# Performance work log

Measured on AMD Instinct MI355X. Metric: run time of the kernel, lower is better.

## Reference

```python
import jax, jax.numpy as jnp
import numpy as np
from jax import lax

N_LAYERS = 10
N_BLOCKS = 3
N_STACK = N_LAYERS * N_BLOCKS  # 30
WIDTH = 512
SKIP_W = 256
CH = 1
QUANT = 256
BOTTLENECK = 16
KSIZE = 3
SCALE = 2 ** (N_LAYERS - 1)  # 512, nearest upsample factor
B, T = 1, 16384
T_EMB = T // SCALE  # 32


def causal_conv(x, w, b, dilation):
    # x: [B,Cin,T], w: [Cout,Cin,K] -> causal dilated conv, output [B,Cout,T]
    k = w.shape[-1]
    pad = (k - 1) * dilation
    y = lax.conv_general_dilated(x, w, window_strides=(1,), padding=[(pad, 0)],
                                 rhs_dilation=(dilation,),
                                 dimension_numbers=('NCH', 'OIH', 'NCH'))
    return y + b[None, :, None]


def conv1x1(x, w, b):
    # x: [B,Cin,T], w: [Cout,Cin]
    return jnp.einsum('oc,bct->bot', w, x) + b[None, :, None]


def setup_inputs() -> dict:
    key = jax.random.key(0)
    ks = jax.random.split(key, 24)
    s = 0.05
    inp = {
        'x': jax.random.normal(ks[0], (B, CH, T), jnp.float32),
        'embedding': jax.random.normal(ks[1], (B, BOTTLENECK, T_EMB), jnp.float32),
        'w_init': jax.random.normal(ks[2], (WIDTH, CH, KSIZE), jnp.float32) * s,
        'b_init': jnp.zeros((WIDTH,), jnp.float32),
        'w_iskip': jax.random.normal(ks[3], (SKIP_W, WIDTH), jnp.float32) * s,
        'b_iskip': jnp.zeros((SKIP_W,), jnp.float32),
        'w_dil': jax.random.normal(ks[4], (N_STACK, 2 * WIDTH, WIDTH, KSIZE), jnp.float32) * s,
        'b_dil': jnp.zeros((N_STACK, 2 * WIDTH), jnp.float32),
        'w_cond': jax.random.normal(ks[5], (N_STACK, 2 * WIDTH, BOTTLENECK), jnp.float32) * s,
        'b_cond': jnp.zeros((N_STACK, 2 * WIDTH), jnp.float32),
        'w_res': jax.random.normal(ks[6], (N_STACK, WIDTH, WIDTH), jnp.float32) * s,
        'b_res': jnp.zeros((N_STACK, WIDTH), jnp.float32),
        'w_skip': jax.random.normal(ks[7], (N_STACK, SKIP_W, WIDTH), jnp.float32) * s,
        'b_skip': jnp.zeros((N_STACK, SKIP_W), jnp.float32),
        'w_fskip': jax.random.normal(ks[8], (SKIP_W, SKIP_W), jnp.float32) * s,
        'b_fskip': jnp.zeros((SKIP_W,), jnp.float32),
        'w_fcond': jax.random.normal(ks[9], (SKIP_W, BOTTLENECK), jnp.float32) * s,
        'b_fcond': jnp.zeros((SKIP_W,), jnp.float32),
        'w_quant': jax.random.normal(ks[10], (QUANT, SKIP_W), jnp.float32) * s,
        'b_quant': jnp.zeros((QUANT,), jnp.float32),
    }
    return inp


def reference(x, embedding, w_init, b_init, w_iskip, b_iskip, w_dil, b_dil,
              w_cond, b_cond, w_res, b_res, w_skip, b_skip,
              w_fskip, b_fskip, w_fcond, b_fcond, w_quant, b_quant):
    # initial causal conv (kernel 3, dilation 1) + initial skip 1x1
    h = causal_conv(x, w_init, b_init, 1)            # [B,WIDTH,T]
    skip = conv1x1(h, w_iskip, b_iskip)              # [B,SKIP_W,T]
    for i in range(N_STACK):
        dilation = 2 ** (i % N_LAYERS)
        cond = conv1x1(embedding, w_cond[i], b_cond[i])      # [B,2W,T_EMB]
        cond_up = jnp.repeat(cond, SCALE, axis=-1)           # nearest upsample -> [B,2W,T]
        dilated = causal_conv(h, w_dil[i], b_dil[i], dilation) + cond_up
        filters = jax.nn.sigmoid(dilated[:, :WIDTH, :])
        gates = jnp.tanh(dilated[:, WIDTH:, :])
        pre = filters * gates
        h = h + conv1x1(pre, w_res[i], b_res[i])
        skip = skip + conv1x1(pre, w_skip[i], b_skip[i])
    skip = conv1x1(jax.nn.relu(skip), w_fskip, b_fskip)
    fcond = jnp.repeat(conv1x1(embedding, w_fcond, b_fcond), SCALE, axis=-1)
    skip = skip + fcond
    return conv1x1(jax.nn.relu(skip), w_quant, b_quant)     # [B,QUANT,T]
```

## Files before the change

kernel.cpp:

```cpp
#include <hip/hip_runtime.h>


typedef _Float16 f16x8 __attribute__((ext_vector_type(8)));
typedef float f32x4 __attribute__((ext_vector_type(4)));

#define NSTACK 30
#define TLEN   16384

typedef __attribute__((address_space(1))) const unsigned int glob_u32;
typedef __attribute__((address_space(3))) unsigned int lds_u32;

__device__ __forceinline__ void gll16(const unsigned short* g, unsigned short* l) {
  __builtin_amdgcn_global_load_lds((glob_u32*)g, (lds_u32*)l, 16, 0, 0);
}

__device__ __forceinline__ unsigned short f2h(float x) {
  union { _Float16 h; unsigned short u; } c;
  c.h = (_Float16)x;
  return c.u;
}
__device__ __forceinline__ unsigned pack2(float a, float b) {
  return (unsigned)f2h(a) | ((unsigned)f2h(b) << 16);
}
__device__ __forceinline__ float uplo(unsigned u){ union{unsigned v;_Float16 h[2];}c; c.v=u; return (float)c.h[0]; }
__device__ __forceinline__ float uphi(unsigned u){ union{unsigned v;_Float16 h[2];}c; c.v=u; return (float)c.h[1]; }
__device__ __forceinline__ f16x8 ldh(const unsigned short* p) {
  return *(const f16x8*)p;
}
__device__ __forceinline__ float sigmoidf_(float x){ return 1.0f/(1.0f+__expf(-x)); }
__device__ __forceinline__ float tanhf_(float x){ return 1.0f - 2.0f/(__expf(2.0f*x)+1.0f); }
#define MFMA16(a,b,c) __builtin_amdgcn_mfma_f32_16x16x32_f16((a),(b),(c),0,0,0)

#define SEG_T  15728640L
#define SEG_R  1966080L
#define SEG_S  983040L
#define SEG_I  32768L
#define SEG_F  16384L
#define SEG_Q  16384L
#define SEG_C  30976L
#define PREP_TOTAL (SEG_T+SEG_R+SEG_S+SEG_I+SEG_F+SEG_Q+SEG_C)

__device__ __forceinline__ void cast4(const float* src, unsigned short* dst, long g){
  f32x4 v = *(const f32x4*)(src + 4*g);
  unsigned int* d = (unsigned int*)(dst + 4*g);
  d[0] = pack2(v[0], v[1]);
  d[1] = pack2(v[2], v[3]);
}

__global__ void prep_kernel(
    const float* __restrict__ w_dil,  unsigned short* __restrict__ A_dil,
    const float* __restrict__ w_res,  unsigned short* __restrict__ Wres_h,
    const float* __restrict__ w_skip, unsigned short* __restrict__ Wskip_h,
    const float* __restrict__ w_iskip,unsigned short* __restrict__ Wiskip_h,
    const float* __restrict__ w_fskip,unsigned short* __restrict__ Wfskip_h,
    const float* __restrict__ w_quant,unsigned short* __restrict__ Wquant_h,
    const float* __restrict__ emb,
    const float* __restrict__ w_cond, const float* __restrict__ b_cond,
    const float* __restrict__ b_dil,
    const float* __restrict__ w_fcond,const float* __restrict__ b_fcond,
    float* __restrict__ cond_all, float* __restrict__ fcond_all) {
  long g = (long)blockIdx.x*256 + threadIdx.x;
  if (g < SEG_T) {
    int c = (int)(g & 511);
    int m = (int)((g >> 9) & 1023);
    int i = (int)(g >> 19);
    const float* s = w_dil + g*3;
    #pragma unroll
    for (int tap=0; tap<3; ++tap)
      A_dil[(((size_t)i*3+tap)*1024 + m)*512 + c] = f2h(s[tap]);
    return;
  }
  g -= SEG_T;
  if (g < SEG_R) { cast4(w_res,  Wres_h,  g); return; }
  g -= SEG_R;
  if (g < SEG_S) { cast4(w_skip, Wskip_h, g); return; }
  g -= SEG_S;
  if (g < SEG_I) { cast4(w_iskip, Wiskip_h, g); return; }
  g -= SEG_I;
  if (g < SEG_F) { cast4(w_fskip, Wfskip_h, g); return; }
  g -= SEG_F;
  if (g < SEG_Q) { cast4(w_quant, Wquant_h, g); return; }
  g -= SEG_Q;
  if (g < NSTACK*1024) {
    int row = (int)g;
    float acc[32];
    float base = b_cond[row] + b_dil[row];
    #pragma unroll
    for (int e=0;e<32;++e) acc[e] = base;
    #pragma unroll
    for (int c=0;c<16;++c) {
      float wv = w_cond[(size_t)row*16 + c];
      #pragma unroll
      for (int e=0;e<32;++e) acc[e] += wv * emb[c*32+e];
    }
    #pragma unroll
    for (int e=0;e<32;++e) cond_all[(size_t)row*32+e] = acc[e];
  } else if (g < NSTACK*1024 + 256) {
    int m = (int)(g - NSTACK*1024);
    float acc[32];
    float base = b_fcond[m];
    #pragma unroll
    for (int c=0;c<16;++c) {
      float wv = w_fcond[(size_t)m*16 + c];
      #pragma unroll
      for (int e=0;e<32;++e) acc[e] = (c==0 ? base : acc[e]) + wv * emb[c*32+e];
    }
    #pragma unroll
    for (int e=0;e<32;++e) fcond_all[(size_t)m*32+e] = acc[e];
  }
}

__global__ __launch_bounds__(512) void hs_kernel(
    const float* __restrict__ x, const float* __restrict__ w_init,
    const float* __restrict__ b_init,
    unsigned short* __restrict__ h_h16,
    const unsigned short* __restrict__ Wiskip,
    const float* __restrict__ b_iskip, unsigned short* __restrict__ skip16) {
  __shared__ unsigned short S[64][520];
  const int tid = threadIdx.x;
  const int tb = blockIdx.x << 6;

  for (int j = tid; j < 64*128; j += 512) {
    int r  = j >> 7;
    int c4 = (j & 127) << 2;
    int t  = tb + r;
    float xm2 = (t>=2)? x[t-2] : 0.f;
    float xm1 = (t>=1)? x[t-1] : 0.f;
    float x0  = x[t];
    float hv[4];
    #pragma unroll
    for (int q=0;q<4;++q) {
      int cc = c4 + q;
      hv[q] = w_init[cc*3+0]*xm2 + w_init[cc*3+1]*xm1 + w_init[cc*3+2]*x0 + b_init[cc];
    }
    unsigned p0 = pack2(hv[0],hv[1]), p1 = pack2(hv[2],hv[3]);
    unsigned int* hb = (unsigned int*)&h_h16[(size_t)t*512 + c4];
    hb[0] = p0; hb[1] = p1;
    unsigned int* sb = (unsigned int*)&S[r][c4];
    sb[0] = p0; sb[1] = p1;
  }
  __syncthreads();

  const int w = tid >> 6, l = tid & 63, lr = l & 15, lc = l >> 4;
  f32x4 acc[2][4];
  #pragma unroll
  for (int mf=0;mf<2;++mf)
    #pragma unroll
    for (int nf=0;nf<4;++nf) acc[mf][nf] = {0.f,0.f,0.f,0.f};
  for (int kc=0;kc<512;kc+=32) {
    f16x8 b[4];
    #pragma unroll
    for (int nf=0;nf<4;++nf)
      b[nf] = ldh(&S[16*nf+lr][kc + lc*8]);
    #pragma unroll
    for (int mf=0;mf<2;++mf) {
      f16x8 a = ldh(&Wiskip[(size_t)(w*32+16*mf+lr)*512 + kc + lc*8]);
      #pragma unroll
      for (int nf=0;nf<4;++nf)
        acc[mf][nf] = MFMA16(a, b[nf], acc[mf][nf]);
    }
  }
  #pragma unroll
  for (int mf=0;mf<2;++mf)
    #pragma unroll
    for (int nf=0;nf<4;++nf) {
      int s0 = w*32+16*mf+4*lc;
      int t  = tb+16*nf+lr;
      unsigned int* pp = (unsigned int*)&skip16[(size_t)t*256+s0];
      pp[0] = pack2(acc[mf][nf][0]+b_iskip[s0+0], acc[mf][nf][1]+b_iskip[s0+1]);
      pp[1] = pack2(acc[mf][nf][2]+b_iskip[s0+2], acc[mf][nf][3]+b_iskip[s0+3]);
    }
}

__global__ __launch_bounds__(512, 4) void dil_small_kernel(
    const unsigned short* __restrict__ h_in,
    unsigned short* __restrict__ pre,
    const unsigned short* __restrict__ A_dil,
    const float* __restrict__ cond,
    const unsigned short* __restrict__ zerobuf,
    int dilation) {
  __shared__ unsigned short Ab[2][128][32];
  __shared__ unsigned short Bb[2][384][32];
  const int tid = threadIdx.x;
  const int w = tid >> 6, l = tid & 63;
  const int lr = l & 15, lc = l >> 4;
  const int nt = blockIdx.x & 63, mt = blockIdx.x >> 6;
  const int tb = nt << 8;
  const int e  = tb >> 9;
  const int wr = w >> 2, wc = w & 3;

  const int srowA  = (w<<4) + (l>>2);
  const int srowB0 = w*48 + (l>>2);
  const int schunk = (l & 3) << 3;

  f32x4 fa[2][4], ga[2][4];
  #pragma unroll
  for (int mf=0;mf<2;++mf)
    #pragma unroll
    for (int nf=0;nf<4;++nf) { fa[mf][nf] = {0.f,0.f,0.f,0.f}; ga[mf][nf] = {0.f,0.f,0.f,0.f}; }

  auto stageA = [&](int buf, int s){
    const int kcc = s / 3;
    const int tap = s - kcc*3;
    const int kc  = kcc << 5;
    const int r = srowA;
    const int m = mt*64 + r + ((r>>6)*448);
    gll16(A_dil + (size_t)tap*(1024*512) + (size_t)m*512 + kc + schunk,
          &Ab[buf][(w<<4)][0]);
  };
  auto stageB = [&](int buf, int kcc){
    const int kc = kcc << 5;
    #pragma unroll
    for (int j=0;j<3;++j){
      const int r = srowB0 + j*16;
      const int t = tb + r - 128;
      const unsigned short* src = (t >= 0) ? (h_in + (size_t)t*512 + kc + schunk)
                                           : (zerobuf + schunk);
      gll16(src, &Bb[buf][w*48 + j*16][0]);
    }
  };

  stageA(0, 0);
  stageB(0, 0);
  for (int s=0; s<48; ++s) {
    const int curA = s & 1;
    const int kcc = s / 3;
    const int tap = s - kcc*3;
    const int curB = kcc & 1;
    __syncthreads();
    if (s+1 < 48) stageA(curA^1, s+1);
    if (tap == 2 && kcc+1 < 16) stageB(curB^1, kcc+1);
    const int shift = (2 - tap) * dilation;
    f16x8 af[2], ag[2], bf[4];
    #pragma unroll
    for (int mf=0;mf<2;++mf){
      const int row = (wr<<5) + (mf<<4) + lr;
      af[mf] = ldh(&Ab[curA][row][lc<<3]);
      ag[mf] = ldh(&Ab[curA][64+row][lc<<3]);
    }
    #pragma unroll
    for (int nf=0;nf<4;++nf){
      const int col = (wc<<6) + (nf<<4) + lr;
      bf[nf] = ldh(&Bb[curB][128 + col - shift][lc<<3]);
    }
    #pragma unroll
    for (int mf=0;mf<2;++mf)
      #pragma unroll
      for (int nf=0;nf<4;++nf){
        fa[mf][nf] = MFMA16(af[mf], bf[nf], fa[mf][nf]);
        ga[mf][nf] = MFMA16(ag[mf], bf[nf], ga[mf][nf]);
      }
  }

  #pragma unroll
  for (int mf=0;mf<2;++mf)
    #pragma unroll
    for (int nf=0;nf<4;++nf){
      const int m0 = mt*64 + (wr<<5) + (mf<<4) + (lc<<2);
      const int t  = tb + (wc<<6) + (nf<<4) + lr;
      float pv[4];
      #pragma unroll
      for (int r=0;r<4;++r){
        float f = fa[mf][nf][r] + cond[(size_t)(m0+r)*32 + e];
        float g = ga[mf][nf][r] + cond[(size_t)(m0+r+512)*32 + e];
        pv[r] = sigmoidf_(f) * tanhf_(g);
      }
      unsigned int* pp = (unsigned int*)&pre[(size_t)t*512 + m0];
      pp[0] = pack2(pv[0], pv[1]);
      pp[1] = pack2(pv[2], pv[3]);
    }
}

__global__ __launch_bounds__(512, 4) void dil_kernel(
    const unsigned short* __restrict__ h_in,
    unsigned short* __restrict__ pre,
    const unsigned short* __restrict__ A_dil,
    const float* __restrict__ cond,
    const unsigned short* __restrict__ zerobuf,
    int dilation) {
  __shared__ unsigned short Ab[2][128][32];
  __shared__ unsigned short Bb[2][256][32];
  const int tid = threadIdx.x;
  const int w = tid >> 6, l = tid & 63;
  const int lr = l & 15, lc = l >> 4;
  const int nt = blockIdx.x & 63, mt = blockIdx.x >> 6;
  const int tb = nt << 8;
  const int e  = tb >> 9;
  const int wr = w >> 2, wc = w & 3;

  const int srowA = (w<<4) + (l>>2);
  const int srowB0 = (w<<5) + (l>>2);
  const int schunk = (l & 3) << 3;

  f32x4 fa[2][4], ga[2][4];
  #pragma unroll
  for (int mf=0;mf<2;++mf)
    #pragma unroll
    for (int nf=0;nf<4;++nf) { fa[mf][nf] = {0.f,0.f,0.f,0.f}; ga[mf][nf] = {0.f,0.f,0.f,0.f}; }

  auto stage = [&](int buf, int s){
    const int tap = s >> 4;
    const int kc  = (s & 15) << 5;
    const int shift = (2 - tap) * dilation;
    {
      const int r = srowA;
      const int m = mt*64 + r + ((r>>6)*448);
      gll16(A_dil + (size_t)tap*(1024*512) + (size_t)m*512 + kc + schunk,
            &Ab[buf][(w<<4)][0]);
    }
    #pragma unroll
    for (int j=0;j<2;++j){
      const int r = srowB0 + (j<<4);
      const int t = tb + r - shift;
      const unsigned short* srcB = (t >= 0) ? (h_in + (size_t)t*512 + kc + schunk)
                                            : (zerobuf + schunk);
      gll16(srcB, &Bb[buf][(w<<5)+(j<<4)][0]);
    }
  };

  stage(0, 0);
  for (int s=0; s<48; ++s) {
    const int cur = s & 1;
    __syncthreads();
    if (s+1 < 48) stage(cur^1, s+1);
    f16x8 af[2], ag[2], bf[4];
    #pragma unroll
    for (int mf=0;mf<2;++mf){
      const int row = (wr<<5) + (mf<<4) + lr;
      af[mf] = ldh(&Ab[cur][row][lc<<3]);
      ag[mf] = ldh(&Ab[cur][64+row][lc<<3]);
    }
    #pragma unroll
    for (int nf=0;nf<4;++nf)
      bf[nf] = ldh(&Bb[cur][(wc<<6)+(nf<<4)+lr][lc<<3]);
    #pragma unroll
    for (int mf=0;mf<2;++mf)
      #pragma unroll
      for (int nf=0;nf<4;++nf){
        fa[mf][nf] = MFMA16(af[mf], bf[nf], fa[mf][nf]);
        ga[mf][nf] = MFMA16(ag[mf], bf[nf], ga[mf][nf]);
      }
  }

  #pragma unroll
  for (int mf=0;mf<2;++mf)
    #pragma unroll
    for (int nf=0;nf<4;++nf){
      const int m0 = mt*64 + (wr<<5) + (mf<<4) + (lc<<2);
      const int t  = tb + (wc<<6) + (nf<<4) + lr;
      float pv[4];
      #pragma unroll
      for (int r=0;r<4;++r){
        float f = fa[mf][nf][r] + cond[(size_t)(m0+r)*32 + e];
        float g = ga[mf][nf][r] + cond[(size_t)(m0+r+512)*32 + e];
        pv[r] = sigmoidf_(f) * tanhf_(g);
      }
      unsigned int* pp = (unsigned int*)&pre[(size_t)t*512 + m0];
      pp[0] = pack2(pv[0], pv[1]);
      pp[1] = pack2(pv[2], pv[3]);
    }
}

__global__ __launch_bounds__(512, 4) void ressk_kernel(
    const unsigned short* __restrict__ pre,
    const unsigned short* __restrict__ h_in,
    unsigned short* __restrict__ h_out,
    unsigned short* __restrict__ skip16,
    const unsigned short* __restrict__ Wres,
    const unsigned short* __restrict__ Wskip,
    const float* __restrict__ b_res,
    const float* __restrict__ b_skip) {
  __shared__ unsigned short Ab[2][128][32];
  __shared__ unsigned short Bb[2][256][32];
  const int tid = threadIdx.x;
  const int w = tid >> 6, l = tid & 63;
  const int lr = l & 15, lc = l >> 4;
  const int nt = blockIdx.x & 63, mt = blockIdx.x >> 6;
  const int tb = nt << 8;
  const int wr = w >> 2, wc = w & 3;
  const bool isres = (mt < 4);
  const unsigned short* W = isres ? Wres : Wskip;
  const int mrow0 = (isres ? mt : (mt-4)) * 128;

  const int srowA = (w<<4) + (l>>2);
  const int srowB0 = (w<<5) + (l>>2);
  const int schunk = (l & 3) << 3;

  f32x4 acc[4][4];
  #pragma unroll
  for (int mf=0;mf<4;++mf)
    #pragma unroll
    for (int nf=0;nf<4;++nf) acc[mf][nf] = {0.f,0.f,0.f,0.f};

  auto stage = [&](int buf, int s){
    const int kc = s << 5;
    gll16(W + (size_t)(mrow0 + srowA)*512 + kc + schunk, &Ab[buf][(w<<4)][0]);
    #pragma unroll
    for (int j=0;j<2;++j){
      const int r = srowB0 + (j<<4);
      gll16(pre + (size_t)(tb + r)*512 + kc + schunk, &Bb[buf][(w<<5)+(j<<4)][0]);
    }
  };

  stage(0, 0);
  for (int s=0; s<16; ++s) {
    const int cur = s & 1;
    __syncthreads();
    if (s+1 < 16) stage(cur^1, s+1);
    f16x8 a[4], bf[4];
    #pragma unroll
    for (int mf=0;mf<4;++mf)
      a[mf] = ldh(&Ab[cur][(wr<<6)+(mf<<4)+lr][lc<<3]);
    #pragma unroll
    for (int nf=0;nf<4;++nf)
      bf[nf] = ldh(&Bb[cur][(wc<<6)+(nf<<4)+lr][lc<<3]);
    #pragma unroll
    for (int mf=0;mf<4;++mf)
      #pragma unroll
      for (int nf=0;nf<4;++nf)
        acc[mf][nf] = MFMA16(a[mf], bf[nf], acc[mf][nf]);
  }

  if (isres) {
    #pragma unroll
    for (int mf=0;mf<4;++mf)
      #pragma unroll
      for (int nf=0;nf<4;++nf){
        const int m0 = mrow0 + (wr<<6) + (mf<<4) + (lc<<2);
        const int t  = tb + (wc<<6) + (nf<<4) + lr;
        const unsigned int* hi = (const unsigned int*)&h_in[(size_t)t*512 + m0];
        unsigned int h01 = hi[0], h23 = hi[1];
        float v0 = uplo(h01) + acc[mf][nf][0] + b_res[m0+0];
        float v1 = uphi(h01) + acc[mf][nf][1] + b_res[m0+1];
        float v2 = uplo(h23) + acc[mf][nf][2] + b_res[m0+2];
        float v3 = uphi(h23) + acc[mf][nf][3] + b_res[m0+3];
        unsigned int* hb = (unsigned int*)&h_out[(size_t)t*512 + m0];
        hb[0] = pack2(v0,v1); hb[1] = pack2(v2,v3);
      }
  } else {
    #pragma unroll
    for (int mf=0;mf<4;++mf)
      #pragma unroll
      for (int nf=0;nf<4;++nf){
        const int s0 = mrow0 + (wr<<6) + (mf<<4) + (lc<<2);
        const int t  = tb + (wc<<6) + (nf<<4) + lr;
        unsigned int* sp = (unsigned int*)&skip16[(size_t)t*256 + s0];
        unsigned int s01 = sp[0], s23 = sp[1];
        float v0 = uplo(s01) + acc[mf][nf][0] + b_skip[s0+0];
        float v1 = uphi(s01) + acc[mf][nf][1] + b_skip[s0+1];
        float v2 = uplo(s23) + acc[mf][nf][2] + b_skip[s0+2];
        float v3 = uphi(s23) + acc[mf][nf][3] + b_skip[s0+3];
        sp[0] = pack2(v0,v1); sp[1] = pack2(v2,v3);
      }
  }
}

__global__ __launch_bounds__(512) void final_kernel(
    const unsigned short* __restrict__ skip16, const unsigned short* __restrict__ Wfs,
    const float* __restrict__ b_fskip, const float* __restrict__ fcond,
    const unsigned short* __restrict__ Wq, const float* __restrict__ b_quant,
    float* __restrict__ out) {
  __shared__ unsigned short S1[64][264];
  __shared__ unsigned short S2[64][264];
  int tid=threadIdx.x, w=tid>>6, l=tid&63, lr=l&15, lc=l>>4;
  int tb = blockIdx.x<<6, e = tb>>9;

  for (int j = tid; j < 64*32; j += 512) {
    int r  = j >> 5;
    int c8 = (j & 31) << 3;
    const unsigned int* sp = (const unsigned int*)&skip16[(size_t)(tb+r)*256 + c8];
    unsigned int* dp = (unsigned int*)&S1[r][c8];
    #pragma unroll
    for (int q=0;q<4;++q){
      unsigned int u = sp[q];
      dp[q] = pack2(fmaxf(uplo(u),0.f), fmaxf(uphi(u),0.f));
    }
  }
  __syncthreads();

  f32x4 acc[2][4];
  #pragma unroll
  for (int mf=0;mf<2;++mf)
    #pragma unroll
    for (int nf=0;nf<4;++nf) acc[mf][nf] = {0.f,0.f,0.f,0.f};
  for (int kc=0;kc<256;kc+=32) {
    f16x8 b[4];
    #pragma unroll
    for (int nf=0;nf<4;++nf) b[nf] = ldh(&S1[16*nf+lr][kc + lc*8]);
    #pragma unroll
    for (int mf=0;mf<2;++mf) {
      f16x8 a = ldh(&Wfs[(size_t)(w*32+16*mf+lr)*256 + kc + lc*8]);
      #pragma unroll
      for (int nf=0;nf<4;++nf)
        acc[mf][nf] = MFMA16(a, b[nf], acc[mf][nf]);
    }
  }
  #pragma unroll
  for (int mf=0;mf<2;++mf)
    #pragma unroll
    for (int nf=0;nf<4;++nf) {
      int m0 = w*32+16*mf+4*lc;
      int n  = 16*nf+lr;
      float pv[4];
      #pragma unroll
      for (int r=0;r<4;++r) {
        float v = acc[mf][nf][r] + b_fskip[m0+r] + fcond[(size_t)(m0+r)*32 + e];
        pv[r] = fmaxf(v, 0.f);
      }
      unsigned int* pp = (unsigned int*)&S2[n][m0];
      pp[0] = pack2(pv[0],pv[1]); pp[1] = pack2(pv[2],pv[3]);
    }
  __syncthreads();

  f32x4 acc2[2][4];
  #pragma unroll
  for (int mf=0;mf<2;++mf)
    #pragma unroll
    for (int nf=0;nf<4;++nf) acc2[mf][nf] = {0.f,0.f,0.f,0.f};
  for (int kc=0;kc<256;kc+=32) {
    f16x8 b[4];
    #pragma unroll
    for (int nf=0;nf<4;++nf) b[nf] = ldh(&S2[16*nf+lr][kc + lc*8]);
    #pragma unroll
    for (int mf=0;mf<2;++mf) {
      f16x8 a = ldh(&Wq[(size_t)(w*32+16*mf+lr)*256 + kc + lc*8]);
      #pragma unroll
      for (int nf=0;nf<4;++nf)
        acc2[mf][nf] = MFMA16(a, b[nf], acc2[mf][nf]);
    }
  }
  #pragma unroll
  for (int mf=0;mf<2;++mf)
    #pragma unroll
    for (int nf=0;nf<4;++nf) {
      int q0 = w*32+16*mf+4*lc;
      int t  = tb + 16*nf + lr;
      #pragma unroll
      for (int r=0;r<4;++r)
        out[(size_t)(q0+r)*TLEN + t] = acc2[mf][nf][r] + b_quant[q0+r];
    }
}


extern "C" void kernel_launch(void* const* d_in, const int* in_sizes, int n_in,
                              void* d_out, int out_size, void* d_ws, size_t ws_size,
                              hipStream_t stream) {
  const float* x       = (const float*)d_in[0];
  const float* emb     = (const float*)d_in[1];
  const float* w_init  = (const float*)d_in[2];
  const float* b_init  = (const float*)d_in[3];
  const float* w_iskip = (const float*)d_in[4];
  const float* b_iskip = (const float*)d_in[5];
  const float* w_dil   = (const float*)d_in[6];
  const float* b_dil   = (const float*)d_in[7];
  const float* w_cond  = (const float*)d_in[8];
  const float* b_cond  = (const float*)d_in[9];
  const float* w_res   = (const float*)d_in[10];
  const float* b_res   = (const float*)d_in[11];
  const float* w_skip  = (const float*)d_in[12];
  const float* b_skip  = (const float*)d_in[13];
  const float* w_fskip = (const float*)d_in[14];
  const float* b_fskip = (const float*)d_in[15];
  const float* w_fcond = (const float*)d_in[16];
  const float* b_fcond = (const float*)d_in[17];
  const float* w_quant = (const float*)d_in[18];
  const float* b_quant = (const float*)d_in[19];
  float* out = (float*)d_out;

  char* ws = (char*)d_ws;
  size_t off = 0;
  auto carve = [&](size_t bytes) -> void* {
    void* p = ws + off;
    off += (bytes + 255) & ~(size_t)255;
    return p;
  };
  unsigned short* A_dil     = (unsigned short*)carve((size_t)NSTACK*3*1024*512*2);
  unsigned short* Wres_h    = (unsigned short*)carve((size_t)NSTACK*512*512*2);
  unsigned short* Wskip_h   = (unsigned short*)carve((size_t)NSTACK*256*512*2);
  unsigned short* Wiskip_h  = (unsigned short*)carve((size_t)256*512*2);
  unsigned short* Wfskip_h  = (unsigned short*)carve((size_t)256*256*2);
  unsigned short* Wquant_h  = (unsigned short*)carve((size_t)256*256*2);
  unsigned short* h_h16     = (unsigned short*)carve((size_t)2*TLEN*512*2);
  unsigned short* pre_h16   = (unsigned short*)carve((size_t)TLEN*512*2);
  unsigned short* skip_h16  = (unsigned short*)carve((size_t)TLEN*256*2);
  float*          cond_all  = (float*)carve((size_t)NSTACK*1024*32*4);
  float*          fcond_all = (float*)carve((size_t)256*32*4);
  unsigned short* zerobuf   = (unsigned short*)carve((size_t)512*2);
  if (off > ws_size) return;

  hipMemsetAsync(zerobuf, 0, 512*2, stream);

  prep_kernel<<<(int)(PREP_TOTAL/256), 256, 0, stream>>>(
      w_dil, A_dil, w_res, Wres_h, w_skip, Wskip_h, w_iskip, Wiskip_h,
      w_fskip, Wfskip_h, w_quant, Wquant_h,
      emb, w_cond, b_cond, b_dil, w_fcond, b_fcond, cond_all, fcond_all);

  hs_kernel<<<TLEN/64, 512, 0, stream>>>(
      x, w_init, b_init, h_h16, Wiskip_h, b_iskip, skip_h16);

  const size_t HB = (size_t)TLEN*512;
  for (int i = 0; i < NSTACK; ++i) {
    int d = 1 << (i % 10);
    const unsigned short* h_in = h_h16 + (size_t)(i & 1)*HB;
    unsigned short* h_out      = h_h16 + (size_t)((i + 1) & 1)*HB;
    if (d <= 64) {
      dil_small_kernel<<<512, 512, 0, stream>>>(
          h_in, pre_h16,
          A_dil + (size_t)i*3*1024*512,
          cond_all + (size_t)i*1024*32,
          zerobuf, d);
    } else {
      dil_kernel<<<512, 512, 0, stream>>>(
          h_in, pre_h16,
          A_dil + (size_t)i*3*1024*512,
          cond_all + (size_t)i*1024*32,
          zerobuf, d);
    }
    ressk_kernel<<<384, 512, 0, stream>>>(
        pre_h16, h_in, h_out, skip_h16,
        Wres_h + (size_t)i*512*512,
        Wskip_h + (size_t)i*256*512,
        b_res + (size_t)i*512,
        b_skip + (size_t)i*256);
  }

  final_kernel<<<TLEN/64, 512, 0, stream>>>(
      skip_h16, Wfskip_h, b_fskip, fcond_all, Wquant_h, b_quant, out);
}
```

Measured before the change: 2.819 ms.

## Fuse dilated conv and res/skip kernels into one launch with per-tile flags

Merges the per-layer dilated-conv kernel and the residual/skip kernel into a single launch of 896 blocks. The first 512 blocks compute the gated pre-activations and bump a per-time-tile counter. The remaining 384 blocks spin on that counter until all 8 channel tiles for their time tile are ready, then run the res/skip GEMM. This is meant to overlap the tail of one stage with the start of the next and cut the per-layer launch count in half. It risks deadlock or idle spinning if consumer blocks take CU slots before their producers are scheduled, and the noinline bodies with a shared LDS pool may change register allocation.

```diff
diff --git a/kernel.cpp b/kernel.cpp
--- a/kernel.cpp
+++ b/kernel.cpp
@@ -9,8 +9,13 @@
 
 typedef __attribute__((address_space(1))) const unsigned int glob_u32;
 typedef __attribute__((address_space(3))) unsigned int lds_u32;
+typedef __attribute__((address_space(3))) unsigned short lds_us;
+typedef __attribute__((address_space(3))) const f16x8 lds_f16x8;
 
 __device__ __forceinline__ void gll16(const unsigned short* g, unsigned short* l) {
+  __builtin_amdgcn_global_load_lds((glob_u32*)g, (lds_u32*)l, 16, 0, 0);
+}
+__device__ __forceinline__ void gll16l(const unsigned short* g, lds_us* l) {
   __builtin_amdgcn_global_load_lds((glob_u32*)g, (lds_u32*)l, 16, 0, 0);
 }
 
@@ -27,9 +32,20 @@
 __device__ __forceinline__ f16x8 ldh(const unsigned short* p) {
   return *(const f16x8*)p;
 }
+__device__ __forceinline__ f16x8 ldh3(const lds_us* p) {
+  return *(lds_f16x8*)p;
+}
 __device__ __forceinline__ float sigmoidf_(float x){ return 1.0f/(1.0f+__expf(-x)); }
 __device__ __forceinline__ float tanhf_(float x){ return 1.0f - 2.0f/(__expf(2.0f*x)+1.0f); }
 #define MFMA16(a,b,c) __builtin_amdgcn_mfma_f32_16x16x32_f16((a),(b),(c),0,0,0)
+
+__device__ __forceinline__ void spin_ge(int* p, int v){
+  while (__hip_atomic_load(p, __ATOMIC_ACQUIRE, __HIP_MEMORY_SCOPE_AGENT) < v)
+    __builtin_amdgcn_s_sleep(2);
+}
+__device__ __forceinline__ void flag_add(int* p){
+  __hip_atomic_fetch_add(p, 1, __ATOMIC_RELEASE, __HIP_MEMORY_SCOPE_AGENT);
+}
 
 #define SEG_T  15728640L
 #define SEG_R  1966080L
@@ -172,23 +188,22 @@
     }
 }
 
-__global__ __launch_bounds__(512, 4) void dil_small_kernel(
+
+__device__ __noinline__ void dil_small_body(
+    lds_us* pool,
     const unsigned short* __restrict__ h_in,
     unsigned short* __restrict__ pre,
     const unsigned short* __restrict__ A_dil,
     const float* __restrict__ cond,
     const unsigned short* __restrict__ zerobuf,
-    int dilation) {
-  __shared__ unsigned short Ab[2][128][32];
-  __shared__ unsigned short Bb[2][384][32];
-  const int tid = threadIdx.x;
+    int dilation, int nt, int mt, int tid) {
+  lds_us* Ab = pool;
+  lds_us* Bb = pool + 8192;
   const int w = tid >> 6, l = tid & 63;
   const int lr = l & 15, lc = l >> 4;
-  const int nt = blockIdx.x & 63, mt = blockIdx.x >> 6;
   const int tb = nt << 8;
   const int e  = tb >> 9;
   const int wr = w >> 2, wc = w & 3;
-
   const int srowA  = (w<<4) + (l>>2);
   const int srowB0 = w*48 + (l>>2);
   const int schunk = (l & 3) << 3;
@@ -205,8 +220,8 @@
     const int kc  = kcc << 5;
     const int r = srowA;
     const int m = mt*64 + r + ((r>>6)*448);
-    gll16(A_dil + (size_t)tap*(1024*512) + (size_t)m*512 + kc + schunk,
-          &Ab[buf][(w<<4)][0]);
+    gll16l(A_dil + (size_t)tap*(1024*512) + (size_t)m*512 + kc + schunk,
+           Ab + buf*4096 + (w<<4)*32);
   };
   auto stageB = [&](int buf, int kcc){
     const int kc = kcc << 5;
@@ -216,7 +231,7 @@
       const int t = tb + r - 128;
       const unsigned short* src = (t >= 0) ? (h_in + (size_t)t*512 + kc + schunk)
                                            : (zerobuf + schunk);
-      gll16(src, &Bb[buf][w*48 + j*16][0]);
+      gll16l(src, Bb + buf*12288 + (w*48 + j*16)*32);
     }
   };
 
@@ -235,13 +250,13 @@
     #pragma unroll
     for (int mf=0;mf<2;++mf){
       const int row = (wr<<5) + (mf<<4) + lr;
-      af[mf] = ldh(&Ab[curA][row][lc<<3]);
-      ag[mf] = ldh(&Ab[curA][64+row][lc<<3]);
+      af[mf] = ldh3(Ab + curA*4096 + row*32 + (lc<<3));
+      ag[mf] = ldh3(Ab + curA*4096 + (64+row)*32 + (lc<<3));
     }
     #pragma unroll
     for (int nf=0;nf<4;++nf){
       const int col = (wc<<6) + (nf<<4) + lr;
-      bf[nf] = ldh(&Bb[curB][128 + col - shift][lc<<3]);
+      bf[nf] = ldh3(Bb + curB*12288 + (128 + col - shift)*32 + (lc<<3));
     }
     #pragma unroll
     for (int mf=0;mf<2;++mf)
@@ -271,23 +286,21 @@
     }
 }
 
-__global__ __launch_bounds__(512, 4) void dil_kernel(
+__device__ __noinline__ void dil_big_body(
+    lds_us* pool,
     const unsigned short* __restrict__ h_in,
     unsigned short* __restrict__ pre,
     const unsigned short* __restrict__ A_dil,
     const float* __restrict__ cond,
     const unsigned short* __restrict__ zerobuf,
-    int dilation) {
-  __shared__ unsigned short Ab[2][128][32];
-  __shared__ unsigned short Bb[2][256][32];
-  const int tid = threadIdx.x;
+    int dilation, int nt, int mt, int tid) {
+  lds_us* Ab = pool;
+  lds_us* Bb = pool + 8192;
   const int w = tid >> 6, l = tid & 63;
   const int lr = l & 15, lc = l >> 4;
-  const int nt = blockIdx.x & 63, mt = blockIdx.x >> 6;
   const int tb = nt << 8;
   const int e  = tb >> 9;
   const int wr = w >> 2, wc = w & 3;
-
   const int srowA = (w<<4) + (l>>2);
   const int srowB0 = (w<<5) + (l>>2);
   const int schunk = (l & 3) << 3;
@@ -305,8 +318,8 @@
     {
       const int r = srowA;
       const int m = mt*64 + r + ((r>>6)*448);
-      gll16(A_dil + (size_t)tap*(1024*512) + (size_t)m*512 + kc + schunk,
-            &Ab[buf][(w<<4)][0]);
+      gll16l(A_dil + (size_t)tap*(1024*512) + (size_t)m*512 + kc + schunk,
+             Ab + buf*4096 + (w<<4)*32);
     }
     #pragma unroll
     for (int j=0;j<2;++j){
@@ -314,7 +327,7 @@
       const int t = tb + r - shift;
       const unsigned short* srcB = (t >= 0) ? (h_in + (size_t)t*512 + kc + schunk)
                                             : (zerobuf + schunk);
-      gll16(srcB, &Bb[buf][(w<<5)+(j<<4)][0]);
+      gll16l(srcB, Bb + buf*8192 + ((w<<5)+(j<<4))*32);
     }
   };
 
@@ -327,12 +340,12 @@
     #pragma unroll
     for (int mf=0;mf<2;++mf){
       const int row = (wr<<5) + (mf<<4) + lr;
-      af[mf] = ldh(&Ab[cur][row][lc<<3]);
-      ag[mf] = ldh(&Ab[cur][64+row][lc<<3]);
+      af[mf] = ldh3(Ab + cur*4096 + row*32 + (lc<<3));
+      ag[mf] = ldh3(Ab + cur*4096 + (64+row)*32 + (lc<<3));
     }
     #pragma unroll
     for (int nf=0;nf<4;++nf)
-      bf[nf] = ldh(&Bb[cur][(wc<<6)+(nf<<4)+lr][lc<<3]);
+      bf[nf] = ldh3(Bb + cur*8192 + ((wc<<6)+(nf<<4)+lr)*32 + (lc<<3));
     #pragma unroll
     for (int mf=0;mf<2;++mf)
       #pragma unroll
@@ -361,7 +374,8 @@
     }
 }
 
-__global__ __launch_bounds__(512, 4) void ressk_kernel(
+__device__ __noinline__ void ressk_body(
+    lds_us* pool,
     const unsigned short* __restrict__ pre,
     const unsigned short* __restrict__ h_in,
     unsigned short* __restrict__ h_out,
@@ -369,19 +383,17 @@
     const unsigned short* __restrict__ Wres,
     const unsigned short* __restrict__ Wskip,
     const float* __restrict__ b_res,
-    const float* __restrict__ b_skip) {
-  __shared__ unsigned short Ab[2][128][32];
-  __shared__ unsigned short Bb[2][256][32];
-  const int tid = threadIdx.x;
+    const float* __restrict__ b_skip,
+    int nt, int mt, int tid) {
+  lds_us* Ab = pool;
+  lds_us* Bb = pool + 8192;
   const int w = tid >> 6, l = tid & 63;
   const int lr = l & 15, lc = l >> 4;
-  const int nt = blockIdx.x & 63, mt = blockIdx.x >> 6;
   const int tb = nt << 8;
   const int wr = w >> 2, wc = w & 3;
   const bool isres = (mt < 4);
   const unsigned short* W = isres ? Wres : Wskip;
   const int mrow0 = (isres ? mt : (mt-4)) * 128;
-
   const int srowA = (w<<4) + (l>>2);
   const int srowB0 = (w<<5) + (l>>2);
   const int schunk = (l & 3) << 3;
@@ -394,11 +406,11 @@
 
   auto stage = [&](int buf, int s){
     const int kc = s << 5;
-    gll16(W + (size_t)(mrow0 + srowA)*512 + kc + schunk, &Ab[buf][(w<<4)][0]);
+    gll16l(W + (size_t)(mrow0 + srowA)*512 + kc + schunk, Ab + buf*4096 + (w<<4)*32);
     #pragma unroll
     for (int j=0;j<2;++j){
       const int r = srowB0 + (j<<4);
-      gll16(pre + (size_t)(tb + r)*512 + kc + schunk, &Bb[buf][(w<<5)+(j<<4)][0]);
+      gll16l(pre + (size_t)(tb + r)*512 + kc + schunk, Bb + buf*8192 + ((w<<5)+(j<<4))*32);
     }
   };
 
@@ -410,10 +422,10 @@
     f16x8 a[4], bf[4];
     #pragma unroll
     for (int mf=0;mf<4;++mf)
-      a[mf] = ldh(&Ab[cur][(wr<<6)+(mf<<4)+lr][lc<<3]);
+      a[mf] = ldh3(Ab + cur*4096 + ((wr<<6)+(mf<<4)+lr)*32 + (lc<<3));
     #pragma unroll
     for (int nf=0;nf<4;++nf)
-      bf[nf] = ldh(&Bb[cur][(wc<<6)+(nf<<4)+lr][lc<<3]);
+      bf[nf] = ldh3(Bb + cur*8192 + ((wc<<6)+(nf<<4)+lr)*32 + (lc<<3));
     #pragma unroll
     for (int mf=0;mf<4;++mf)
       #pragma unroll
@@ -453,6 +465,41 @@
         sp[0] = pack2(v0,v1); sp[1] = pack2(v2,v3);
       }
   }
+}
+
+__global__ __launch_bounds__(512, 4) void layer_kernel(
+    const unsigned short* __restrict__ h_in,
+    unsigned short* __restrict__ h_out,
+    unsigned short* __restrict__ pre,
+    unsigned short* __restrict__ skip16,
+    const unsigned short* __restrict__ A_dil,
+    const unsigned short* __restrict__ Wres,
+    const unsigned short* __restrict__ Wskip,
+    const float* __restrict__ cond,
+    const float* __restrict__ b_res,
+    const float* __restrict__ b_skip,
+    const unsigned short* __restrict__ zerobuf,
+    int dilation,
+    int* __restrict__ pre_cnt) {
+  __shared__ unsigned short POOL[32768];
+  lds_us* pool = (lds_us*)POOL;
+  const int tid = threadIdx.x;
+
+  if (blockIdx.x < 512) {
+    const int nt = blockIdx.x & 63, mt = blockIdx.x >> 6;
+    if (dilation <= 64)
+      dil_small_body(pool, h_in, pre, A_dil, cond, zerobuf, dilation, nt, mt, tid);
+    else
+      dil_big_body(pool, h_in, pre, A_dil, cond, zerobuf, dilation, nt, mt, tid);
+    __syncthreads();
+    if (tid == 0){ __threadfence(); flag_add(&pre_cnt[nt]); }
+    return;
+  }
+  const int b2 = blockIdx.x - 512;
+  const int nt = b2 & 63, mt = b2 >> 6;
+  if (tid == 0) spin_ge(&pre_cnt[nt], 8);
+  __syncthreads();
+  ressk_body(pool, pre, h_in, h_out, skip16, Wres, Wskip, b_res, b_skip, nt, mt, tid);
 }
 
 __global__ __launch_bounds__(512) void final_kernel(
@@ -586,9 +633,11 @@
   float*          cond_all  = (float*)carve((size_t)NSTACK*1024*32*4);
   float*          fcond_all = (float*)carve((size_t)256*32*4);
   unsigned short* zerobuf   = (unsigned short*)carve((size_t)512*2);
+  int*            flags     = (int*)carve((size_t)NSTACK*64*4);
   if (off > ws_size) return;
 
   hipMemsetAsync(zerobuf, 0, 512*2, stream);
+  hipMemsetAsync(flags, 0, (size_t)NSTACK*64*4, stream);
 
   prep_kernel<<<(int)(PREP_TOTAL/256), 256, 0, stream>>>(
       w_dil, A_dil, w_res, Wres_h, w_skip, Wskip_h, w_iskip, Wiskip_h,
@@ -603,25 +652,16 @@
     int d = 1 << (i % 10);
     const unsigned short* h_in = h_h16 + (size_t)(i & 1)*HB;
     unsigned short* h_out      = h_h16 + (size_t)((i + 1) & 1)*HB;
-    if (d <= 64) {
-      dil_small_kernel<<<512, 512, 0, stream>>>(
-          h_in, pre_h16,
-          A_dil + (size_t)i*3*1024*512,
-          cond_all + (size_t)i*1024*32,
-          zerobuf, d);
-    } else {
-      dil_kernel<<<512, 512, 0, stream>>>(
-          h_in, pre_h16,
-          A_dil + (size_t)i*3*1024*512,
-          cond_all + (size_t)i*1024*32,
-          zerobuf, d);
-    }
-    ressk_kernel<<<384, 512, 0, stream>>>(
-        pre_h16, h_in, h_out, skip_h16,
+    layer_kernel<<<896, 512, 0, stream>>>(
+        h_in, h_out, pre_h16, skip_h16,
+        A_dil + (size_t)i*3*1024*512,
         Wres_h + (size_t)i*512*512,
         Wskip_h + (size_t)i*256*512,
+        cond_all + (size_t)i*1024*32,
         b_res + (size_t)i*512,
-        b_skip + (size_t)i*256);
+        b_skip + (size_t)i*256,
+        zerobuf, d,
+        flags + (size_t)i*64);
   }
 
   final_kernel<<<TLEN/64, 512, 0, stream>>>(
```

New measurement: 5.161 ms. 1.83x slower.
